# Kernel optimization log

Hardware: AMD Instinct MI355X
Metric: run time of the kernel (lower is better)

## Reference

```python
import jax, jax.numpy as jnp
import numpy as np

B, T, H = 256, 512, 256


def setup_inputs() -> dict:
    key = jax.random.key(0)
    ks = jax.random.split(key, 16)
    s_in, s_h = 1.0 / np.sqrt(1.0), 1.0 / np.sqrt(H)

    def u(k, shape, s):
        return jax.random.uniform(k, shape, jnp.float32, -s, s)

    return {
        "x": jax.random.normal(ks[0], (B, T), jnp.float32),
        # LSTMCell 1: input size 1
        "W_ih1": u(ks[1], (4 * H, 1), s_h), "b_ih1": u(ks[2], (4 * H,), s_h),
        "W_hh1": u(ks[3], (4 * H, H), s_h), "b_hh1": u(ks[4], (4 * H,), s_h),
        # LSTMCell 2: input size H
        "W_ih2": u(ks[5], (4 * H, H), s_h), "b_ih2": u(ks[6], (4 * H,), s_h),
        "W_hh2": u(ks[7], (4 * H, H), s_h), "b_hh2": u(ks[8], (4 * H,), s_h),
        # SelfAttention linears
        "Wa1": u(ks[9], (H, H), s_h), "ba1": u(ks[10], (H,), s_h),
        "Wa2": u(ks[11], (H, H), s_h), "ba2": u(ks[12], (H,), s_h),
        # output linear H -> 1
        "Wo": u(ks[13], (1, H), s_h), "bo": u(ks[14], (1,), s_h),
        "future": 0,
    }


def _lstm_cell(h, c, gates):
    i, f, g, o = jnp.split(gates, 4, axis=-1)
    i, f, o = jax.nn.sigmoid(i), jax.nn.sigmoid(f), jax.nn.sigmoid(o)
    g = jnp.tanh(g)
    c = f * c + i * g
    return o * jnp.tanh(c), c


def reference(x, W_ih1, b_ih1, W_hh1, b_hh1, W_ih2, b_ih2, W_hh2, b_hh2,
              Wa1, ba1, Wa2, ba2, Wo, bo, future):
    n, Tt = x.shape
    Hd = W_hh1.shape[1]

    def step_core(h1, c1, h2, c2, x_t):
        # x_t: [B, 1]
        g1 = x_t @ W_ih1.T + b_ih1 + h1 @ W_hh1.T + b_hh1
        h1, c1 = _lstm_cell(h1, c1, g1)
        g2 = h1 @ W_ih2.T + b_ih2 + h2 @ W_hh2.T + b_hh2
        h2, c2 = _lstm_cell(h2, c2, g2)
        # additive self-attention (dropout p=0 -> identity)
        attn = jax.nn.softmax(jnp.tanh(h2 @ Wa1.T + ba1) @ Wa2.T + ba2, axis=-1)
        out = (attn * h2) @ Wo.T + bo  # [B, 1]
        return h1, c1, h2, c2, out

    def step(carry, x_t):
        h1, c1, h2, c2, _ = carry
        h1, c1, h2, c2, out = step_core(h1, c1, h2, c2, x_t)
        return (h1, c1, h2, c2, out), out

    z = jnp.zeros((n, Hd), x.dtype)
    init = (z, z, z, z, jnp.zeros((n, 1), x.dtype))
    xs = x.T[:, :, None]  # [T, B, 1]
    carry, outs = jax.lax.scan(step, init, xs)

    if future > 0:
        def fstep(carry, _):
            h1, c1, h2, c2, out = carry
            h1, c1, h2, c2, out = step_core(h1, c1, h2, c2, out)
            return (h1, c1, h2, c2, out), out
        _, fouts = jax.lax.scan(fstep, carry, None, length=future)
        outs = jnp.concatenate([outs, fouts], axis=0)

    return outs[:, :, 0].T  # [B, T+future]
```

## Files before the change

kernel.cpp:

```cpp
#include <hip/hip_runtime.h>
#include <hip/hip_bf16.h>

#define HD   256
#define TT   512

typedef unsigned short u16;
typedef unsigned int   u32;
typedef unsigned long long u64;
typedef __attribute__((ext_vector_type(8))) short  short8;
typedef __attribute__((ext_vector_type(4))) float  f32x4;

__device__ __forceinline__ float bf2f(u16 v) { return __uint_as_float(((u32)v) << 16); }
__device__ __forceinline__ u16 f2bf(float f) {
    u32 u = __float_as_uint(f);
    u32 r = u + 0x7fffu + ((u >> 16) & 1u);
    return (u16)(r >> 16);
}
__device__ __forceinline__ float sigf(float x)  { return __builtin_amdgcn_rcpf(1.f + __expf(-x)); }
__device__ __forceinline__ float tanhf_(float x){ float e = __expf(-2.f * x);
                                                  return 2.f * __builtin_amdgcn_rcpf(1.f + e) - 1.f; }

__global__ void cvt_bf_kernel(const float* __restrict__ src, u16* __restrict__ dst, int n) {
    int idx = blockIdx.x * 256 + threadIdx.x;
    if (idx < n) dst[idx] = f2bf(src[idx]);
}

__global__ void bias_kernel(const float* __restrict__ a1, const float* __restrict__ b1,
                            const float* __restrict__ a2, const float* __restrict__ b2,
                            float* __restrict__ o1, float* __restrict__ o2) {
    int i = blockIdx.x * 256 + threadIdx.x;
    o1[i] = a1[i] + b1[i];
    o2[i] = a2[i] + b2[i];
}

__device__ __forceinline__ void load_bfrag(const float* __restrict__ W, int row, int kq, short8* bw) {
#pragma unroll
    for (int kk = 0; kk < 8; ++kk) {
        const float* p = W + row * 256 + kk * 32 + kq * 8;
        short8 s;
#pragma unroll
        for (int j = 0; j < 8; ++j) s[j] = (short)f2bf(p[j]);
        bw[kk] = s;
    }
}

__device__ __forceinline__ u64 aload64(const u64* p) {
    return __hip_atomic_load(p, __ATOMIC_RELAXED, __HIP_MEMORY_SCOPE_AGENT);
}
__device__ __forceinline__ void astore32(u32* p, u32 v) {
    __hip_atomic_store(p, v, __ATOMIC_RELAXED, __HIP_MEMORY_SCOPE_AGENT);
}

__device__ __forceinline__ void flag_wait(const u32* flags, int gb, u32 target) {
    if (threadIdx.x < 8) {
        const u32* slot = flags + (gb * 8 + (int)threadIdx.x) * 32;
        int sp = 0;
        while (__hip_atomic_load(slot, __ATOMIC_RELAXED, __HIP_MEMORY_SCOPE_AGENT) < target) {
            if (++sp > (1 << 24)) break;
        }
    }
    __syncthreads();
}

__device__ __forceinline__ void flag_post(u32* flags, int slotidx, u32 val) {
    __syncthreads();
    if (threadIdx.x == 0)
        __hip_atomic_store(flags + slotidx * 32, val, __ATOMIC_RELAXED, __HIP_MEMORY_SCOPE_AGENT);
}

__global__ __launch_bounds__(512) void lstm_persist(
    const float* __restrict__ x,
    const float* __restrict__ Wih1,
    const float* __restrict__ bias1,
    const float* __restrict__ bias2,
    const float* __restrict__ Whh1,
    const float* __restrict__ Wih2,
    const float* __restrict__ Whh2,
    u32* __restrict__ Hb1, u32* __restrict__ Hb2,
    u16* __restrict__ H2out, u32* flags)
{
    __shared__ __align__(16) u16 sh1hi[16 * 264], sh1lo[16 * 264];
    __shared__ __align__(16) u16 sh2hi[16 * 264], sh2lo[16 * 264];
    __shared__ float xs[TT * 16];
    __shared__ float gbuf1[4 * 16 * 36], gbuf2[4 * 16 * 36];
    __shared__ float wihs[128], b1s[128], b2s[128];

    const int tid = threadIdx.x;
    const int blk = blockIdx.x;
    const int gb = (blk & 7) + ((blk >> 6) << 3);
    const int hg = (blk >> 3) & 7;
    const int l = tid & 63, wv = tid >> 6;
    const int g = wv >> 1, hh = wv & 1;
    const int nloc = l & 15, kq = l >> 4;
    const int wrow = g * 256 + hg * 32 + hh * 16 + nloc;

    short8 bW1[8], bW2[8], bW3[8];
    load_bfrag(Whh1, wrow, kq, bW1);
    load_bfrag(Wih2, wrow, kq, bW2);
    load_bfrag(Whh2, wrow, kq, bW3);

    for (int idx = tid; idx < 16 * TT; idx += 512) {
        int b = idx >> 9, t = idx & 511;
        xs[t * 16 + b] = x[(gb * 16 + b) * TT + t];
    }
    if (tid < 128) {
        int rr = (tid >> 5) * 256 + hg * 32 + (tid & 31);
        wihs[tid] = Wih1[rr]; b1s[tid] = bias1[rr]; b2s[tid] = bias2[rr];
    }

    const int cb = tid >> 5, ci = tid & 31;
    const int bg = gb * 16 + cb, ig = hg * 32 + ci;
#pragma unroll
    for (int pp = 0; pp < 2; ++pp) {
        astore32(&Hb1[((pp * 256 + bg) << 8) + ig], 0u);
        astore32(&Hb2[((pp * 256 + bg) << 8) + ig], 0u);
    }
    float c1 = 0.f, c2 = 0.f;

    flag_post(flags, gb * 8 + hg, 1u);

    const int aoff = nloc * 264 + kq * 8;
    const int sb = tid >> 5, scol = (tid & 31) * 8;
    const int sbase = sb * 264 + scol;

    for (int k = 0; k <= TT; ++k) {
        flag_wait(flags, gb, (u32)(k + 1));

        const int rp = k & 1, wp = rp ^ 1;
        {
            const u32* p1 = Hb1 + ((rp * 256 + gb * 16 + sb) << 8) + scol;
            const u32* p2 = Hb2 + ((rp * 256 + gb * 16 + sb) << 8) + scol;
            u32 w1v[8], w2v[8];
#pragma unroll
            for (int j = 0; j < 4; ++j) {
                u64 t = aload64((const u64*)p1 + j);
                w1v[2 * j] = (u32)t; w1v[2 * j + 1] = (u32)(t >> 32);
            }
#pragma unroll
            for (int j = 0; j < 4; ++j) {
                u64 t = aload64((const u64*)p2 + j);
                w2v[2 * j] = (u32)t; w2v[2 * j + 1] = (u32)(t >> 32);
            }
            u32 h1h[4], h1l[4], h2h[4], h2l[4];
#pragma unroll
            for (int i = 0; i < 4; ++i) {
                u32 a = w1v[2 * i], b = w1v[2 * i + 1];
                h1h[i] = (a & 0xffffu) | (b << 16);
                h1l[i] = (a >> 16) | (b & 0xffff0000u);
                a = w2v[2 * i]; b = w2v[2 * i + 1];
                h2h[i] = (a & 0xffffu) | (b << 16);
                h2l[i] = (a >> 16) | (b & 0xffff0000u);
            }
            *(uint4*)(sh1hi + sbase) = *(uint4*)(h1h);
            *(uint4*)(sh1lo + sbase) = *(uint4*)(h1l);
            *(uint4*)(sh2hi + sbase) = *(uint4*)(h2h);
            *(uint4*)(sh2lo + sbase) = *(uint4*)(h2l);
        }
        __syncthreads();

        f32x4 acc1a = {0,0,0,0}, acc1b = {0,0,0,0};
        f32x4 acc2a = {0,0,0,0}, acc2b = {0,0,0,0};
#pragma unroll
        for (int kk = 0; kk < 8; ++kk) {
            short8 a1h = *(const short8*)(sh1hi + aoff + kk * 32);
            short8 a1l = *(const short8*)(sh1lo + aoff + kk * 32);
            if (k < TT) {
                acc1a = __builtin_amdgcn_mfma_f32_16x16x32_bf16(a1h, bW1[kk], acc1a, 0, 0, 0);
                acc1b = __builtin_amdgcn_mfma_f32_16x16x32_bf16(a1l, bW1[kk], acc1b, 0, 0, 0);
            }
            if (k > 0) {
                acc2a = __builtin_amdgcn_mfma_f32_16x16x32_bf16(a1h, bW2[kk], acc2a, 0, 0, 0);
                acc2b = __builtin_amdgcn_mfma_f32_16x16x32_bf16(a1l, bW2[kk], acc2b, 0, 0, 0);
                short8 a2h = *(const short8*)(sh2hi + aoff + kk * 32);
                short8 a2l = *(const short8*)(sh2lo + aoff + kk * 32);
                acc2a = __builtin_amdgcn_mfma_f32_16x16x32_bf16(a2h, bW3[kk], acc2a, 0, 0, 0);
                acc2b = __builtin_amdgcn_mfma_f32_16x16x32_bf16(a2l, bW3[kk], acc2b, 0, 0, 0);
            }
        }
#pragma unroll
        for (int r = 0; r < 4; ++r) {
            int m = (l >> 4) * 4 + r;
            gbuf1[(g * 16 + m) * 36 + hh * 16 + nloc] = acc1a[r] + acc1b[r];
            gbuf2[(g * 16 + m) * 36 + hh * 16 + nloc] = acc2a[r] + acc2b[r];
        }
        __syncthreads();

        u16 hi2 = 0;
        if (k < TT) {
            float xv = xs[k * 16 + cb];
            float g0 = gbuf1[(0 * 16 + cb) * 36 + ci] + xv * wihs[ci]      + b1s[ci];
            float g1 = gbuf1[(1 * 16 + cb) * 36 + ci] + xv * wihs[32 + ci] + b1s[32 + ci];
            float g2 = gbuf1[(2 * 16 + cb) * 36 + ci] + xv * wihs[64 + ci] + b1s[64 + ci];
            float g3 = gbuf1[(3 * 16 + cb) * 36 + ci] + xv * wihs[96 + ci] + b1s[96 + ci];
            float ii = sigf(g0), ff = sigf(g1), gg = tanhf_(g2), oo = sigf(g3);
            c1 = ff * c1 + ii * gg;
            float h = oo * tanhf_(c1);
            u16 hi = f2bf(h); u32 word = (u32)hi | ((u32)f2bf(h - bf2f(hi)) << 16);
            astore32(&Hb1[((wp * 256 + bg) << 8) + ig], word);
        }
        if (k > 0) {
            float g0 = gbuf2[(0 * 16 + cb) * 36 + ci] + b2s[ci];
            float g1 = gbuf2[(1 * 16 + cb) * 36 + ci] + b2s[32 + ci];
            float g2 = gbuf2[(2 * 16 + cb) * 36 + ci] + b2s[64 + ci];
            float g3 = gbuf2[(3 * 16 + cb) * 36 + ci] + b2s[96 + ci];
            float ii = sigf(g0), ff = sigf(g1), gg = tanhf_(g2), oo = sigf(g3);
            c2 = ff * c2 + ii * gg;
            float h = oo * tanhf_(c2);
            hi2 = f2bf(h); u32 word = (u32)hi2 | ((u32)f2bf(h - bf2f(hi2)) << 16);
            astore32(&Hb2[((wp * 256 + bg) << 8) + ig], word);
        }
        flag_post(flags, gb * 8 + hg, (u32)(k + 2));
        if (k > 0) H2out[(bg * TT + (k - 1)) * 256 + ig] = hi2;
    }
}

__global__ __launch_bounds__(256) void attn_fused(
    const u16*  __restrict__ Wa1b, const u16* __restrict__ Wa2b,
    const float* __restrict__ ba1, const float* __restrict__ ba2,
    const float* __restrict__ Wo,  const float* __restrict__ bo,
    const u16*  __restrict__ H2,   float* __restrict__ out)
{
    __shared__ __align__(16) u16 sA[64 * 264];
    __shared__ __align__(16) u16 sP[64 * 264];
    __shared__ float red[64 * 12];
    __shared__ float sb1[256], sb2[256], swo[256];

    const int tid = threadIdx.x;
    const int w = tid >> 6, l = tid & 63;
    const int c = l & 15, q = l >> 4;
    const int row0 = blockIdx.x * 64;

    {
        const int r = tid >> 2, qq = tid & 3;
        const uint4* src = (const uint4*)(H2 + (row0 + r) * 256 + qq * 64);
#pragma unroll
        for (int j = 0; j < 8; ++j) {
            uint4 v = src[j];
            *(uint4*)(sA + r * 264 + qq * 64 + j * 8) = v;
        }
    }
    if (tid < 256) { sb1[tid] = ba1[tid]; sb2[tid] = ba2[tid]; swo[tid] = Wo[tid]; }
    __syncthreads();

    f32x4 acc[4][4];
#pragma unroll
    for (int mi = 0; mi < 4; ++mi)
#pragma unroll
        for (int ni = 0; ni < 4; ++ni) acc[mi][ni] = (f32x4){0,0,0,0};

#pragma unroll
    for (int ni = 0; ni < 4; ++ni) {
        const int row = w * 64 + ni * 16 + c;
        const u16* wp = Wa1b + row * 256 + q * 8;
        short8 bW[8];
#pragma unroll
        for (int kk = 0; kk < 8; ++kk) bW[kk] = *(const short8*)(wp + kk * 32);
#pragma unroll
        for (int kk = 0; kk < 8; ++kk)
#pragma unroll
            for (int mi = 0; mi < 4; ++mi) {
                short8 a = *(const short8*)(sA + (mi * 16 + c) * 264 + q * 8 + kk * 32);
                acc[mi][ni] = __builtin_amdgcn_mfma_f32_16x16x32_bf16(a, bW[kk], acc[mi][ni], 0, 0, 0);
            }
    }
#pragma unroll
    for (int mi = 0; mi < 4; ++mi)
#pragma unroll
        for (int ni = 0; ni < 4; ++ni) {
            const int n = w * 64 + ni * 16 + c;
            const float bj = sb1[n];
#pragma unroll
            for (int r = 0; r < 4; ++r) {
                int m = mi * 16 + q * 4 + r;
                sP[m * 264 + n] = f2bf(tanhf(acc[mi][ni][r] + bj));
            }
        }
    __syncthreads();

#pragma unroll
    for (int mi = 0; mi < 4; ++mi)
#pragma unroll
        for (int ni = 0; ni < 4; ++ni) acc[mi][ni] = (f32x4){0,0,0,0};
#pragma unroll
    for (int ni = 0; ni < 4; ++ni) {
        const int row = w * 64 + ni * 16 + c;
        const u16* wp = Wa2b + row * 256 + q * 8;
        short8 bW[8];
#pragma unroll
        for (int kk = 0; kk < 8; ++kk) bW[kk] = *(const short8*)(wp + kk * 32);
#pragma unroll
        for (int kk = 0; kk < 8; ++kk)
#pragma unroll
            for (int mi = 0; mi < 4; ++mi) {
                short8 a = *(const short8*)(sP + (mi * 16 + c) * 264 + q * 8 + kk * 32);
                acc[mi][ni] = __builtin_amdgcn_mfma_f32_16x16x32_bf16(a, bW[kk], acc[mi][ni], 0, 0, 0);
            }
    }

    float mx[4][4];
#pragma unroll
    for (int mi = 0; mi < 4; ++mi)
#pragma unroll
        for (int r = 0; r < 4; ++r) mx[mi][r] = -1e30f;
#pragma unroll
    for (int mi = 0; mi < 4; ++mi)
#pragma unroll
        for (int ni = 0; ni < 4; ++ni) {
            const float bj = sb2[w * 64 + ni * 16 + c];
#pragma unroll
            for (int r = 0; r < 4; ++r) {
                float s = acc[mi][ni][r] + bj;
                acc[mi][ni][r] = s;
                mx[mi][r] = fmaxf(mx[mi][r], s);
            }
        }
#pragma unroll
    for (int off = 1; off < 16; off <<= 1)
#pragma unroll
        for (int mi = 0; mi < 4; ++mi)
#pragma unroll
            for (int r = 0; r < 4; ++r) mx[mi][r] = fmaxf(mx[mi][r], __shfl_xor(mx[mi][r], off));
    if (c == 0)
#pragma unroll
        for (int mi = 0; mi < 4; ++mi)
#pragma unroll
            for (int r = 0; r < 4; ++r) red[(mi * 16 + q * 4 + r) * 12 + w] = mx[mi][r];
    __syncthreads();
#pragma unroll
    for (int mi = 0; mi < 4; ++mi)
#pragma unroll
        for (int r = 0; r < 4; ++r) {
            const float* rp = red + (mi * 16 + q * 4 + r) * 12;
            mx[mi][r] = fmaxf(fmaxf(rp[0], rp[1]), fmaxf(rp[2], rp[3]));
        }
    float suml[4][4], sumw[4][4];
#pragma unroll
    for (int mi = 0; mi < 4; ++mi)
#pragma unroll
        for (int r = 0; r < 4; ++r) { suml[mi][r] = 0.f; sumw[mi][r] = 0.f; }
#pragma unroll
    for (int mi = 0; mi < 4; ++mi)
#pragma unroll
        for (int ni = 0; ni < 4; ++ni) {
            const int n = w * 64 + ni * 16 + c;
            const float wov = swo[n];
#pragma unroll
            for (int r = 0; r < 4; ++r) {
                int m = mi * 16 + q * 4 + r;
                float e = __expf(acc[mi][ni][r] - mx[mi][r]);
                suml[mi][r] += e;
                sumw[mi][r] += e * bf2f(sA[m * 264 + n]) * wov;
            }
        }
#pragma unroll
    for (int off = 1; off < 16; off <<= 1)
#pragma unroll
        for (int mi = 0; mi < 4; ++mi)
#pragma unroll
            for (int r = 0; r < 4; ++r) {
                suml[mi][r] += __shfl_xor(suml[mi][r], off);
                sumw[mi][r] += __shfl_xor(sumw[mi][r], off);
            }
    __syncthreads();
    if (c == 0)
#pragma unroll
        for (int mi = 0; mi < 4; ++mi)
#pragma unroll
            for (int r = 0; r < 4; ++r) {
                int m = mi * 16 + q * 4 + r;
                red[m * 12 + 4 + w] = suml[mi][r];
                red[m * 12 + 8 + w] = sumw[mi][r];
            }
    __syncthreads();
    if (tid < 64) {
        const float* rp = red + tid * 12;
        float lsum = rp[4] + rp[5] + rp[6] + rp[7];
        float wsum = rp[8] + rp[9] + rp[10] + rp[11];
        out[row0 + tid] = wsum / lsum + bo[0];
    }
}

extern "C" void kernel_launch(void* const* d_in, const int* in_sizes, int n_in,
                              void* d_out, int out_size, void* d_ws, size_t ws_size,
                              hipStream_t stream) {
    const float* x    = (const float*)d_in[0];
    const float* Wih1 = (const float*)d_in[1];
    const float* bih1 = (const float*)d_in[2];
    const float* Whh1 = (const float*)d_in[3];
    const float* bhh1 = (const float*)d_in[4];
    const float* Wih2 = (const float*)d_in[5];
    const float* bih2 = (const float*)d_in[6];
    const float* Whh2 = (const float*)d_in[7];
    const float* bhh2 = (const float*)d_in[8];
    const float* Wa1  = (const float*)d_in[9];
    const float* ba1  = (const float*)d_in[10];
    const float* Wa2  = (const float*)d_in[11];
    const float* ba2  = (const float*)d_in[12];
    const float* Wo   = (const float*)d_in[13];
    const float* bo   = (const float*)d_in[14];

    char* ws = (char*)d_ws;
    u16*   Wa1b  = (u16*)(ws + 0);
    u16*   Wa2b  = (u16*)(ws + 131072);
    float* bias1 = (float*)(ws + 262144);
    float* bias2 = (float*)(ws + 266240);
    u32*   flags = (u32*)(ws + 270336);
    u32*   Hb1   = (u32*)(ws + 524288);
    u32*   Hb2   = (u32*)(ws + 1048576);
    u16*   H2    = (u16*)(ws + 2097152);
    float* out   = (float*)d_out;

    (void)hipMemsetAsync(flags, 0, 16384, stream);
    bias_kernel<<<4, 256, 0, stream>>>(bih1, bhh1, bih2, bhh2, bias1, bias2);
    cvt_bf_kernel<<<256, 256, 0, stream>>>(Wa1, Wa1b, 65536);
    cvt_bf_kernel<<<256, 256, 0, stream>>>(Wa2, Wa2b, 65536);

    lstm_persist<<<128, 512, 0, stream>>>(x, Wih1, bias1, bias2,
                                          Whh1, Wih2, Whh2, Hb1, Hb2, H2, flags);
    attn_fused<<<2048, 256, 0, stream>>>(Wa1b, Wa2b, ba1, ba2, Wo, bo, H2, out);
}
```

Before: 2.008 ms.

## Replace flag barriers with step-tagged hidden-state words and drop prep kernels

```diff
diff --git a/kernel.cpp b/kernel.cpp
--- a/kernel.cpp
+++ b/kernel.cpp
@@ -20,19 +20,6 @@
 __device__ __forceinline__ float tanhf_(float x){ float e = __expf(-2.f * x);
                                                   return 2.f * __builtin_amdgcn_rcpf(1.f + e) - 1.f; }
 
-__global__ void cvt_bf_kernel(const float* __restrict__ src, u16* __restrict__ dst, int n) {
-    int idx = blockIdx.x * 256 + threadIdx.x;
-    if (idx < n) dst[idx] = f2bf(src[idx]);
-}
-
-__global__ void bias_kernel(const float* __restrict__ a1, const float* __restrict__ b1,
-                            const float* __restrict__ a2, const float* __restrict__ b2,
-                            float* __restrict__ o1, float* __restrict__ o2) {
-    int i = blockIdx.x * 256 + threadIdx.x;
-    o1[i] = a1[i] + b1[i];
-    o2[i] = a2[i] + b2[i];
-}
-
 __device__ __forceinline__ void load_bfrag(const float* __restrict__ W, int row, int kq, short8* bw) {
 #pragma unroll
     for (int kk = 0; kk < 8; ++kk) {
@@ -47,37 +34,20 @@
 __device__ __forceinline__ u64 aload64(const u64* p) {
     return __hip_atomic_load(p, __ATOMIC_RELAXED, __HIP_MEMORY_SCOPE_AGENT);
 }
-__device__ __forceinline__ void astore32(u32* p, u32 v) {
+__device__ __forceinline__ void astore64(u64* p, u64 v) {
     __hip_atomic_store(p, v, __ATOMIC_RELAXED, __HIP_MEMORY_SCOPE_AGENT);
-}
-
-__device__ __forceinline__ void flag_wait(const u32* flags, int gb, u32 target) {
-    if (threadIdx.x < 8) {
-        const u32* slot = flags + (gb * 8 + (int)threadIdx.x) * 32;
-        int sp = 0;
-        while (__hip_atomic_load(slot, __ATOMIC_RELAXED, __HIP_MEMORY_SCOPE_AGENT) < target) {
-            if (++sp > (1 << 24)) break;
-        }
-    }
-    __syncthreads();
-}
-
-__device__ __forceinline__ void flag_post(u32* flags, int slotidx, u32 val) {
-    __syncthreads();
-    if (threadIdx.x == 0)
-        __hip_atomic_store(flags + slotidx * 32, val, __ATOMIC_RELAXED, __HIP_MEMORY_SCOPE_AGENT);
 }
 
 __global__ __launch_bounds__(512) void lstm_persist(
     const float* __restrict__ x,
     const float* __restrict__ Wih1,
-    const float* __restrict__ bias1,
-    const float* __restrict__ bias2,
+    const float* __restrict__ bih1, const float* __restrict__ bhh1,
+    const float* __restrict__ bih2, const float* __restrict__ bhh2,
     const float* __restrict__ Whh1,
     const float* __restrict__ Wih2,
     const float* __restrict__ Whh2,
-    u32* __restrict__ Hb1, u32* __restrict__ Hb2,
-    u16* __restrict__ H2out, u32* flags)
+    u64* __restrict__ Hb1, u64* __restrict__ Hb2,
+    u16* __restrict__ H2out)
 {
     __shared__ __align__(16) u16 sh1hi[16 * 264], sh1lo[16 * 264];
     __shared__ __align__(16) u16 sh2hi[16 * 264], sh2lo[16 * 264];
@@ -105,49 +75,51 @@
     }
     if (tid < 128) {
         int rr = (tid >> 5) * 256 + hg * 32 + (tid & 31);
-        wihs[tid] = Wih1[rr]; b1s[tid] = bias1[rr]; b2s[tid] = bias2[rr];
+        wihs[tid] = Wih1[rr];
+        b1s[tid] = bih1[rr] + bhh1[rr];
+        b2s[tid] = bih2[rr] + bhh2[rr];
     }
 
     const int cb = tid >> 5, ci = tid & 31;
     const int bg = gb * 16 + cb, ig = hg * 32 + ci;
-#pragma unroll
-    for (int pp = 0; pp < 2; ++pp) {
-        astore32(&Hb1[((pp * 256 + bg) << 8) + ig], 0u);
-        astore32(&Hb2[((pp * 256 + bg) << 8) + ig], 0u);
-    }
     float c1 = 0.f, c2 = 0.f;
-
-    flag_post(flags, gb * 8 + hg, 1u);
 
     const int aoff = nloc * 264 + kq * 8;
     const int sb = tid >> 5, scol = (tid & 31) * 8;
     const int sbase = sb * 264 + scol;
 
     for (int k = 0; k <= TT; ++k) {
-        flag_wait(flags, gb, (u32)(k + 1));
-
         const int rp = k & 1, wp = rp ^ 1;
+
+        const u64* p1 = Hb1 + ((rp * 256 + gb * 16 + sb) << 8) + scol;
+        const u64* p2 = Hb2 + ((rp * 256 + gb * 16 + sb) << 8) + scol;
+        u64 v1[8], v2[8];
         {
-            const u32* p1 = Hb1 + ((rp * 256 + gb * 16 + sb) << 8) + scol;
-            const u32* p2 = Hb2 + ((rp * 256 + gb * 16 + sb) << 8) + scol;
-            u32 w1v[8], w2v[8];
-#pragma unroll
-            for (int j = 0; j < 4; ++j) {
-                u64 t = aload64((const u64*)p1 + j);
-                w1v[2 * j] = (u32)t; w1v[2 * j + 1] = (u32)(t >> 32);
-            }
-#pragma unroll
-            for (int j = 0; j < 4; ++j) {
-                u64 t = aload64((const u64*)p2 + j);
-                w2v[2 * j] = (u32)t; w2v[2 * j + 1] = (u32)(t >> 32);
-            }
+            const u32 tgt = (u32)k;
+            int sp = 0;
+            bool ok;
+            do {
+                ok = true;
+#pragma unroll
+                for (int j = 0; j < 8; ++j) {
+                    v1[j] = aload64(p1 + j);
+                    ok = ok && ((u32)(v1[j] >> 32) >= tgt);
+                }
+#pragma unroll
+                for (int j = 0; j < 8; ++j) {
+                    v2[j] = aload64(p2 + j);
+                    ok = ok && ((u32)(v2[j] >> 32) >= tgt);
+                }
+            } while (!ok && ++sp < (1 << 22));
+        }
+        {
             u32 h1h[4], h1l[4], h2h[4], h2l[4];
 #pragma unroll
             for (int i = 0; i < 4; ++i) {
-                u32 a = w1v[2 * i], b = w1v[2 * i + 1];
+                u32 a = (u32)v1[2 * i], b = (u32)v1[2 * i + 1];
                 h1h[i] = (a & 0xffffu) | (b << 16);
                 h1l[i] = (a >> 16) | (b & 0xffff0000u);
-                a = w2v[2 * i]; b = w2v[2 * i + 1];
+                a = (u32)v2[2 * i]; b = (u32)v2[2 * i + 1];
                 h2h[i] = (a & 0xffffu) | (b << 16);
                 h2l[i] = (a >> 16) | (b & 0xffff0000u);
             }
@@ -185,6 +157,7 @@
         }
         __syncthreads();
 
+        const u64 tagw = (u64)(u32)(k + 1) << 32;
         u16 hi2 = 0;
         if (k < TT) {
             float xv = xs[k * 16 + cb];
@@ -195,8 +168,9 @@
             float ii = sigf(g0), ff = sigf(g1), gg = tanhf_(g2), oo = sigf(g3);
             c1 = ff * c1 + ii * gg;
             float h = oo * tanhf_(c1);
-            u16 hi = f2bf(h); u32 word = (u32)hi | ((u32)f2bf(h - bf2f(hi)) << 16);
-            astore32(&Hb1[((wp * 256 + bg) << 8) + ig], word);
+            u16 hi = f2bf(h);
+            u32 word = (u32)hi | ((u32)f2bf(h - bf2f(hi)) << 16);
+            astore64(&Hb1[((wp * 256 + bg) << 8) + ig], (u64)word | tagw);
         }
         if (k > 0) {
             float g0 = gbuf2[(0 * 16 + cb) * 36 + ci] + b2s[ci];
@@ -206,16 +180,18 @@
             float ii = sigf(g0), ff = sigf(g1), gg = tanhf_(g2), oo = sigf(g3);
             c2 = ff * c2 + ii * gg;
             float h = oo * tanhf_(c2);
-            hi2 = f2bf(h); u32 word = (u32)hi2 | ((u32)f2bf(h - bf2f(hi2)) << 16);
-            astore32(&Hb2[((wp * 256 + bg) << 8) + ig], word);
-        }
-        flag_post(flags, gb * 8 + hg, (u32)(k + 2));
+            hi2 = f2bf(h);
+            u32 word = (u32)hi2 | ((u32)f2bf(h - bf2f(hi2)) << 16);
+            astore64(&Hb2[((wp * 256 + bg) << 8) + ig], (u64)word | tagw);
+        } else {
+            astore64(&Hb2[((wp * 256 + bg) << 8) + ig], tagw);
+        }
         if (k > 0) H2out[(bg * TT + (k - 1)) * 256 + ig] = hi2;
     }
 }
 
 __global__ __launch_bounds__(256) void attn_fused(
-    const u16*  __restrict__ Wa1b, const u16* __restrict__ Wa2b,
+    const float* __restrict__ Wa1, const float* __restrict__ Wa2,
     const float* __restrict__ ba1, const float* __restrict__ ba2,
     const float* __restrict__ Wo,  const float* __restrict__ bo,
     const u16*  __restrict__ H2,   float* __restrict__ out)
@@ -251,10 +227,16 @@
 #pragma unroll
     for (int ni = 0; ni < 4; ++ni) {
         const int row = w * 64 + ni * 16 + c;
-        const u16* wp = Wa1b + row * 256 + q * 8;
+        const float* wpf = Wa1 + row * 256 + q * 8;
         short8 bW[8];
 #pragma unroll
-        for (int kk = 0; kk < 8; ++kk) bW[kk] = *(const short8*)(wp + kk * 32);
+        for (int kk = 0; kk < 8; ++kk) {
+            const float* pp = wpf + kk * 32;
+            short8 s;
+#pragma unroll
+            for (int j = 0; j < 8; ++j) s[j] = (short)f2bf(pp[j]);
+            bW[kk] = s;
+        }
 #pragma unroll
         for (int kk = 0; kk < 8; ++kk)
 #pragma unroll
@@ -284,10 +266,16 @@
 #pragma unroll
     for (int ni = 0; ni < 4; ++ni) {
         const int row = w * 64 + ni * 16 + c;
-        const u16* wp = Wa2b + row * 256 + q * 8;
+        const float* wpf = Wa2 + row * 256 + q * 8;
         short8 bW[8];
 #pragma unroll
-        for (int kk = 0; kk < 8; ++kk) bW[kk] = *(const short8*)(wp + kk * 32);
+        for (int kk = 0; kk < 8; ++kk) {
+            const float* pp = wpf + kk * 32;
+            short8 s;
+#pragma unroll
+            for (int j = 0; j < 8; ++j) s[j] = (short)f2bf(pp[j]);
+            bW[kk] = s;
+        }
 #pragma unroll
         for (int kk = 0; kk < 8; ++kk)
 #pragma unroll
@@ -400,22 +388,14 @@
     const float* bo   = (const float*)d_in[14];
 
     char* ws = (char*)d_ws;
-    u16*   Wa1b  = (u16*)(ws + 0);
-    u16*   Wa2b  = (u16*)(ws + 131072);
-    float* bias1 = (float*)(ws + 262144);
-    float* bias2 = (float*)(ws + 266240);
-    u32*   flags = (u32*)(ws + 270336);
-    u32*   Hb1   = (u32*)(ws + 524288);
-    u32*   Hb2   = (u32*)(ws + 1048576);
-    u16*   H2    = (u16*)(ws + 2097152);
-    float* out   = (float*)d_out;
-
-    (void)hipMemsetAsync(flags, 0, 16384, stream);
-    bias_kernel<<<4, 256, 0, stream>>>(bih1, bhh1, bih2, bhh2, bias1, bias2);
-    cvt_bf_kernel<<<256, 256, 0, stream>>>(Wa1, Wa1b, 65536);
-    cvt_bf_kernel<<<256, 256, 0, stream>>>(Wa2, Wa2b, 65536);
-
-    lstm_persist<<<128, 512, 0, stream>>>(x, Wih1, bias1, bias2,
-                                          Whh1, Wih2, Whh2, Hb1, Hb2, H2, flags);
-    attn_fused<<<2048, 256, 0, stream>>>(Wa1b, Wa2b, ba1, ba2, Wo, bo, H2, out);
-}
+    u64* Hb1 = (u64*)(ws + 0);
+    u64* Hb2 = (u64*)(ws + 1048576);
+    u16* H2  = (u16*)(ws + 2097152);
+    float* out = (float*)d_out;
+
+    (void)hipMemsetAsync(ws, 0, 2097152, stream);
+
+    lstm_persist<<<128, 512, 0, stream>>>(x, Wih1, bih1, bhh1, bih2, bhh2,
+                                          Whh1, Wih2, Whh2, Hb1, Hb2, H2);
+    attn_fused<<<2048, 256, 0, stream>>>(Wa1, Wa2, ba1, ba2, Wo, bo, H2, out);
+}
```

After: 2.874 ms. +43.2%, slower.
